# Optimization experiments

Measured on AMD Instinct MI355X. Metric: run time of the kernel, lower is better.

Reference implementation:

```python
import jax, jax.numpy as jnp
import numpy as np

N_EXPERTS = 8
TOP_K = 2
AUX_LOSS_COEF = 0.01
D_MODEL = 2048


def setup_inputs() -> dict:
    key = jax.random.key(0)
    k1, k2 = jax.random.split(key)
    hidden_states = jax.random.normal(k1, (4, 4096, D_MODEL), dtype=jnp.float32)
    # nn.Linear(d_model, n_experts, bias=False): weight [n_experts, d_model]
    W = jax.random.normal(k2, (N_EXPERTS, D_MODEL), dtype=jnp.float32) * (1.0 / np.sqrt(D_MODEL))
    return {"hidden_states": hidden_states, "W": W}


def reference(hidden_states, W):
    # Flatten [B, S, d] -> [N, d]
    hidden = hidden_states.reshape(-1, hidden_states.shape[-1])
    n_tokens = hidden.shape[0]

    # Gate linear + softmax (eval mode: no jitter noise)
    logits = jnp.einsum("nd,ed->ne", hidden, W)  # [N, E]
    probs = jax.nn.softmax(logits, axis=-1)

    # Top-k routing
    top_probs, top_indices = jax.lax.top_k(probs, TOP_K)  # [N, K]

    # Load distribution via scatter-add (segment_sum over expert ids)
    counts = jax.ops.segment_sum(
        jnp.ones((n_tokens * TOP_K,), dtype=hidden.dtype),
        top_indices.reshape(-1),
        num_segments=N_EXPERTS,
    )
    load = counts / (n_tokens * TOP_K)

    # Aux loss: coefficient of variation squared of the load
    mean_load = load.mean()
    variance = ((load - mean_load) ** 2).mean()
    cv_sq = variance / (mean_load ** 2 + 1e-9)
    aux_loss = AUX_LOSS_COEF * cv_sq

    return top_indices, top_probs, aux_loss, load
```

## Files before the change

kernel.cpp:

```cpp
#include <hip/hip_runtime.h>

#define D_MODEL 2048
#define N_EXP 8
#define TOPK 2
#define TPB 64
#define SPLIT 4
#define KQ (D_MODEL / SPLIT)
#define TILE 64
#define NT (KQ / TILE)
#define TSTR 65
#define OSTR 68

__global__ __launch_bounds__(512, 8) void gate_partial_kernel(
    const float* __restrict__ H, const float* __restrict__ W,
    float* __restrict__ part_ws, int n_tokens)
{
    __shared__ float lbuf[2][TILE][TSTR];

    const int tid = threadIdx.x;
    const int lane = tid & 63;
    const int w = tid >> 6;
    const int tb = blockIdx.x >> 2;
    const int q = blockIdx.x & 3;
    const int t0 = tb * TPB;
    const int wc = __builtin_amdgcn_readfirstlane(w);

    const int srow = tid >> 3;
    const int scol = tid & 7;
    const bool svalid = (t0 + srow) < n_tokens;
    const float4* hrow = reinterpret_cast<const float4*>(H)
                         + (size_t)(t0 + srow) * (D_MODEL / 4) + q * (KQ / 4);
    const float* Wq = W + q * KQ;
    const float4 fz = make_float4(0.f, 0.f, 0.f, 0.f);

    float acc[N_EXP];
#pragma unroll
    for (int e = 0; e < N_EXP; ++e) acc[e] = 0.f;

    {
        float4 r0 = svalid ? hrow[scol] : fz;
        float4 r1 = svalid ? hrow[scol + 8] : fz;
        const float* p0 = reinterpret_cast<const float*>(&r0);
        const float* p1 = reinterpret_cast<const float*>(&r1);
#pragma unroll
        for (int jj = 0; jj < 4; ++jj) {
            lbuf[0][4 * scol + jj][srow] = p0[jj];
            lbuf[0][4 * (scol + 8) + jj][srow] = p1[jj];
        }
    }
    __syncthreads();

#pragma unroll
    for (int j = 0; j < NT; ++j) {
        const int b = j & 1;
        const bool pf = (j + 1 < NT);
        float4 r0 = fz, r1 = fz;
        if (pf && svalid) {
            r0 = hrow[(j + 1) * 16 + scol];
            r1 = hrow[(j + 1) * 16 + scol + 8];
        }

        float x[8];
#pragma unroll
        for (int i = 0; i < 8; ++i) x[i] = lbuf[b][wc * 8 + i][lane];
#pragma unroll
        for (int e = 0; e < N_EXP; ++e) {
            float a = acc[e];
#pragma unroll
            for (int i = 0; i < 8; ++i)
                a = fmaf(x[i], Wq[e * D_MODEL + j * TILE + wc * 8 + i], a);
            acc[e] = a;
        }

        if (pf) {
            const float* p0 = reinterpret_cast<const float*>(&r0);
            const float* p1 = reinterpret_cast<const float*>(&r1);
#pragma unroll
            for (int jj = 0; jj < 4; ++jj) {
                lbuf[b ^ 1][4 * scol + jj][srow] = p0[jj];
                lbuf[b ^ 1][4 * (scol + 8) + jj][srow] = p1[jj];
            }
        }
        __syncthreads();
    }

    float* part = &lbuf[0][0][0];
    {
        float* dst = part + lane * OSTR + wc * 8;
        *reinterpret_cast<float4*>(dst) = make_float4(acc[0], acc[1], acc[2], acc[3]);
        *reinterpret_cast<float4*>(dst + 4) = make_float4(acc[4], acc[5], acc[6], acc[7]);
    }
    __syncthreads();

    if (w == 0 && (t0 + lane) < n_tokens) {
        const float* src = part + lane * OSTR;
        float4 s0 = *reinterpret_cast<const float4*>(src);
        float4 s1 = *reinterpret_cast<const float4*>(src + 4);
        float lg[N_EXP] = {s0.x, s0.y, s0.z, s0.w, s1.x, s1.y, s1.z, s1.w};
#pragma unroll
        for (int c = 1; c < 8; ++c) {
            float4 c0 = *reinterpret_cast<const float4*>(src + c * 8);
            float4 c1 = *reinterpret_cast<const float4*>(src + c * 8 + 4);
            lg[0] += c0.x; lg[1] += c0.y; lg[2] += c0.z; lg[3] += c0.w;
            lg[4] += c1.x; lg[5] += c1.y; lg[6] += c1.z; lg[7] += c1.w;
        }
        float* dst = part_ws + ((size_t)q * n_tokens + (t0 + lane)) * 8;
        *reinterpret_cast<float4*>(dst) = make_float4(lg[0], lg[1], lg[2], lg[3]);
        *reinterpret_cast<float4*>(dst + 4) = make_float4(lg[4], lg[5], lg[6], lg[7]);
    }
}

__global__ __launch_bounds__(512) void token_finalize_kernel(
    const float* __restrict__ part_ws,
    float* __restrict__ out_idx, float* __restrict__ out_prob,
    unsigned int* __restrict__ hist_blk, int n_tokens)
{
    __shared__ unsigned int hist[N_EXP];
    const int tid = threadIdx.x;
    if (tid < N_EXP) hist[tid] = 0u;
    __syncthreads();

    const int t = blockIdx.x * 512 + tid;
    if (t < n_tokens) {
        float lg[N_EXP] = {0.f, 0.f, 0.f, 0.f, 0.f, 0.f, 0.f, 0.f};
#pragma unroll
        for (int qq = 0; qq < SPLIT; ++qq) {
            const float4* src = reinterpret_cast<const float4*>(
                part_ws + ((size_t)qq * n_tokens + t) * 8);
            const float4 a0 = src[0], a1 = src[1];
            lg[0] += a0.x; lg[1] += a0.y; lg[2] += a0.z; lg[3] += a0.w;
            lg[4] += a1.x; lg[5] += a1.y; lg[6] += a1.z; lg[7] += a1.w;
        }

        float m = lg[0];
#pragma unroll
        for (int e = 1; e < N_EXP; ++e) m = fmaxf(m, lg[e]);
        float p[N_EXP], s = 0.f;
#pragma unroll
        for (int e = 0; e < N_EXP; ++e) { p[e] = expf(lg[e] - m); s += p[e]; }
        const float inv = 1.f / s;

        float v1 = -INFINITY, v2 = -INFINITY;
        int i1 = 0, i2 = 0;
#pragma unroll
        for (int e = 0; e < N_EXP; ++e) {
            float vv = lg[e];
            if (vv > v1) { v2 = v1; i2 = i1; v1 = vv; i1 = e; }
            else if (vv > v2) { v2 = vv; i2 = e; }
        }

        *reinterpret_cast<float2*>(&out_idx[2 * t]) = make_float2((float)i1, (float)i2);
        *reinterpret_cast<float2*>(&out_prob[2 * t]) = make_float2(p[i1] * inv, p[i2] * inv);
        atomicAdd(&hist[i1], 1u);
        atomicAdd(&hist[i2], 1u);
    }

    __syncthreads();
    if (tid < N_EXP) hist_blk[blockIdx.x * N_EXP + tid] = hist[tid];
}

__global__ void finalize_kernel(const unsigned int* __restrict__ hist_blk, int nblk,
                                float* __restrict__ out_aux,
                                float* __restrict__ out_load, int n_tokens)
{
    __shared__ float red[256];
    const int tid = threadIdx.x;
    const int e = tid & 7, g = tid >> 3;
    unsigned int s = 0;
    for (int j = g; j < nblk; j += 32) s += hist_blk[j * N_EXP + e];
    red[tid] = (float)s;
    __syncthreads();
#pragma unroll
    for (int st = 128; st >= 8; st >>= 1) {
        if (tid < st) red[tid] += red[tid + st];
        __syncthreads();
    }
    if (tid == 0) {
        const float denom = 1.0f / (float)(n_tokens * TOPK);
        float load[N_EXP], sum = 0.f;
        for (int k = 0; k < N_EXP; ++k) { load[k] = red[k] * denom; sum += load[k]; }
        const float mean = sum / (float)N_EXP;
        float var = 0.f;
        for (int k = 0; k < N_EXP; ++k) { float d = load[k] - mean; var += d * d; }
        var /= (float)N_EXP;
        const float cv_sq = var / (mean * mean + 1e-9f);
        out_aux[0] = 0.01f * cv_sq;
        for (int k = 0; k < N_EXP; ++k) out_load[k] = load[k];
    }
}

extern "C" void kernel_launch(void* const* d_in, const int* in_sizes, int n_in,
                              void* d_out, int out_size, void* d_ws, size_t ws_size,
                              hipStream_t stream)
{
    const float* H = (const float*)d_in[0];
    const float* W = (const float*)d_in[1];
    const int n_tokens = in_sizes[0] / D_MODEL;

    float* out = (float*)d_out;
    float* out_idx = out;
    float* out_prob = out + 2 * (size_t)n_tokens;
    float* out_aux = out + 4 * (size_t)n_tokens;
    float* out_load = out + 4 * (size_t)n_tokens + 1;

    float* part_ws = (float*)d_ws;
    unsigned int* hist_blk = (unsigned int*)((char*)d_ws + (SPLIT * (size_t)n_tokens * 8 * 4));

    const int nblk_t = (n_tokens + TPB - 1) / TPB;
    hipLaunchKernelGGL(gate_partial_kernel, dim3(nblk_t * SPLIT), dim3(512), 0, stream,
                       H, W, part_ws, n_tokens);

    const int nblk_f = (n_tokens + 511) / 512;
    hipLaunchKernelGGL(token_finalize_kernel, dim3(nblk_f), dim3(512), 0, stream,
                       part_ws, out_idx, out_prob, hist_blk, n_tokens);

    hipLaunchKernelGGL(finalize_kernel, dim3(1), dim3(256), 0, stream,
                       hist_blk, nblk_f, out_aux, out_load, n_tokens);
}
```

Measured before the change: 32.93 us.

## Use XOR-swizzled float4 LDS tiles and fuse aux-loss finalize via last-block atomics

The shared-memory tile changes from a padded transposed scalar layout to token-major float4 rows with an XOR swizzle. Stores and loads become 128-bit operations, which cuts the number of LDS instructions per tile while trying to keep bank conflicts low. The separate single-block finalize kernel is also removed. Each finalize block now atomically adds its histogram into a global counter, and the last block to finish computes the load and aux loss. In exchange, a hipMemsetAsync is added to zero the counters each call, and correctness now depends on the threadfence and done-counter ordering.

Result: slower. 40.82 us (+24.0%).

```diff
diff --git a/kernel.cpp b/kernel.cpp
--- a/kernel.cpp
+++ b/kernel.cpp
@@ -8,14 +8,13 @@
 #define KQ (D_MODEL / SPLIT)
 #define TILE 64
 #define NT (KQ / TILE)
-#define TSTR 65
 #define OSTR 68
 
 __global__ __launch_bounds__(512, 8) void gate_partial_kernel(
     const float* __restrict__ H, const float* __restrict__ W,
     float* __restrict__ part_ws, int n_tokens)
 {
-    __shared__ float lbuf[2][TILE][TSTR];
+    __shared__ float4 lbuf[2][TPB][16];
 
     const int tid = threadIdx.x;
     const int lane = tid & 63;
@@ -27,6 +26,7 @@
 
     const int srow = tid >> 3;
     const int scol = tid & 7;
+    const int sw = srow & 15;
     const bool svalid = (t0 + srow) < n_tokens;
     const float4* hrow = reinterpret_cast<const float4*>(H)
                          + (size_t)(t0 + srow) * (D_MODEL / 4) + q * (KQ / 4);
@@ -40,13 +40,8 @@
     {
         float4 r0 = svalid ? hrow[scol] : fz;
         float4 r1 = svalid ? hrow[scol + 8] : fz;
-        const float* p0 = reinterpret_cast<const float*>(&r0);
-        const float* p1 = reinterpret_cast<const float*>(&r1);
-#pragma unroll
-        for (int jj = 0; jj < 4; ++jj) {
-            lbuf[0][4 * scol + jj][srow] = p0[jj];
-            lbuf[0][4 * (scol + 8) + jj][srow] = p1[jj];
-        }
+        lbuf[0][srow][scol ^ sw] = r0;
+        lbuf[0][srow][(scol + 8) ^ sw] = r1;
     }
     __syncthreads();
 
@@ -60,9 +55,10 @@
             r1 = hrow[(j + 1) * 16 + scol + 8];
         }
 
-        float x[8];
-#pragma unroll
-        for (int i = 0; i < 8; ++i) x[i] = lbuf[b][wc * 8 + i][lane];
+        const int lsw = lane & 15;
+        const float4 x0 = lbuf[b][lane][(2 * wc) ^ lsw];
+        const float4 x1 = lbuf[b][lane][(2 * wc + 1) ^ lsw];
+        const float x[8] = {x0.x, x0.y, x0.z, x0.w, x1.x, x1.y, x1.z, x1.w};
 #pragma unroll
         for (int e = 0; e < N_EXP; ++e) {
             float a = acc[e];
@@ -73,18 +69,13 @@
         }
 
         if (pf) {
-            const float* p0 = reinterpret_cast<const float*>(&r0);
-            const float* p1 = reinterpret_cast<const float*>(&r1);
-#pragma unroll
-            for (int jj = 0; jj < 4; ++jj) {
-                lbuf[b ^ 1][4 * scol + jj][srow] = p0[jj];
-                lbuf[b ^ 1][4 * (scol + 8) + jj][srow] = p1[jj];
-            }
+            lbuf[b ^ 1][srow][scol ^ sw] = r0;
+            lbuf[b ^ 1][srow][(scol + 8) ^ sw] = r1;
         }
         __syncthreads();
     }
 
-    float* part = &lbuf[0][0][0];
+    float* part = reinterpret_cast<float*>(&lbuf[0][0][0]);
     {
         float* dst = part + lane * OSTR + wc * 8;
         *reinterpret_cast<float4*>(dst) = make_float4(acc[0], acc[1], acc[2], acc[3]);
@@ -112,12 +103,14 @@
 
 __global__ __launch_bounds__(512) void token_finalize_kernel(
     const float* __restrict__ part_ws,
+    unsigned int* __restrict__ ghist, unsigned int* __restrict__ gdone,
     float* __restrict__ out_idx, float* __restrict__ out_prob,
-    unsigned int* __restrict__ hist_blk, int n_tokens)
+    float* __restrict__ out_aux, float* __restrict__ out_load,
+    int n_tokens, int nblk)
 {
-    __shared__ unsigned int hist[N_EXP];
+    __shared__ unsigned int lhist[N_EXP];
     const int tid = threadIdx.x;
-    if (tid < N_EXP) hist[tid] = 0u;
+    if (tid < N_EXP) lhist[tid] = 0u;
     __syncthreads();
 
     const int t = blockIdx.x * 512 + tid;
@@ -151,41 +144,36 @@
 
         *reinterpret_cast<float2*>(&out_idx[2 * t]) = make_float2((float)i1, (float)i2);
         *reinterpret_cast<float2*>(&out_prob[2 * t]) = make_float2(p[i1] * inv, p[i2] * inv);
-        atomicAdd(&hist[i1], 1u);
-        atomicAdd(&hist[i2], 1u);
-    }
-
-    __syncthreads();
-    if (tid < N_EXP) hist_blk[blockIdx.x * N_EXP + tid] = hist[tid];
-}
-
-__global__ void finalize_kernel(const unsigned int* __restrict__ hist_blk, int nblk,
-                                float* __restrict__ out_aux,
-                                float* __restrict__ out_load, int n_tokens)
-{
-    __shared__ float red[256];
-    const int tid = threadIdx.x;
-    const int e = tid & 7, g = tid >> 3;
-    unsigned int s = 0;
-    for (int j = g; j < nblk; j += 32) s += hist_blk[j * N_EXP + e];
-    red[tid] = (float)s;
-    __syncthreads();
-#pragma unroll
-    for (int st = 128; st >= 8; st >>= 1) {
-        if (tid < st) red[tid] += red[tid + st];
-        __syncthreads();
-    }
+        atomicAdd(&lhist[i1], 1u);
+        atomicAdd(&lhist[i2], 1u);
+    }
+
+    __syncthreads();
+    if (tid < N_EXP) atomicAdd(&ghist[tid], lhist[tid]);
+    __syncthreads();
+
     if (tid == 0) {
-        const float denom = 1.0f / (float)(n_tokens * TOPK);
-        float load[N_EXP], sum = 0.f;
-        for (int k = 0; k < N_EXP; ++k) { load[k] = red[k] * denom; sum += load[k]; }
-        const float mean = sum / (float)N_EXP;
-        float var = 0.f;
-        for (int k = 0; k < N_EXP; ++k) { float d = load[k] - mean; var += d * d; }
-        var /= (float)N_EXP;
-        const float cv_sq = var / (mean * mean + 1e-9f);
-        out_aux[0] = 0.01f * cv_sq;
-        for (int k = 0; k < N_EXP; ++k) out_load[k] = load[k];
+        __threadfence();
+        unsigned int old = atomicAdd(gdone, 1u);
+        if (old == (unsigned int)(nblk - 1)) {
+            const float denom = 1.0f / (float)(n_tokens * TOPK);
+            float load[N_EXP], sum = 0.f;
+#pragma unroll
+            for (int e = 0; e < N_EXP; ++e) {
+                unsigned int c = atomicAdd(&ghist[e], 0u);
+                load[e] = (float)c * denom;
+                sum += load[e];
+            }
+            const float mean = sum / (float)N_EXP;
+            float var = 0.f;
+#pragma unroll
+            for (int e = 0; e < N_EXP; ++e) { float d = load[e] - mean; var += d * d; }
+            var /= (float)N_EXP;
+            const float cv_sq = var / (mean * mean + 1e-9f);
+            out_aux[0] = 0.01f * cv_sq;
+#pragma unroll
+            for (int e = 0; e < N_EXP; ++e) out_load[e] = load[e];
+        }
     }
 }
 
@@ -204,7 +192,11 @@
     float* out_load = out + 4 * (size_t)n_tokens + 1;
 
     float* part_ws = (float*)d_ws;
-    unsigned int* hist_blk = (unsigned int*)((char*)d_ws + (SPLIT * (size_t)n_tokens * 8 * 4));
+    const size_t part_bytes = (size_t)SPLIT * n_tokens * 8 * sizeof(float);
+    unsigned int* ghist = (unsigned int*)((char*)d_ws + part_bytes);
+    unsigned int* gdone = ghist + N_EXP;
+
+    hipMemsetAsync(ghist, 0, (N_EXP + 1) * sizeof(unsigned int), stream);
 
     const int nblk_t = (n_tokens + TPB - 1) / TPB;
     hipLaunchKernelGGL(gate_partial_kernel, dim3(nblk_t * SPLIT), dim3(512), 0, stream,
@@ -212,8 +204,6 @@
 
     const int nblk_f = (n_tokens + 511) / 512;
     hipLaunchKernelGGL(token_finalize_kernel, dim3(nblk_f), dim3(512), 0, stream,
-                       part_ws, out_idx, out_prob, hist_blk, n_tokens);
-
-    hipLaunchKernelGGL(finalize_kernel, dim3(1), dim3(256), 0, stream,
-                       hist_blk, nblk_f, out_aux, out_load, n_tokens);
+                       part_ws, ghist, gdone,
+                       out_idx, out_prob, out_aux, out_load, n_tokens, nblk_f);
 }
```
